# Performance work log

Hardware: AMD Instinct MI355X
Metric: run time of the kernel (lower is better)

## Reference

```python
import jax, jax.numpy as jnp
import numpy as np

# dims / config (from init_kwargs)
B, N, D, H = 8, 512, 256, 8
M, K, R = 8, 16, 8            # n_slots basis graphs, slot_dim, kernel_rank
DH = D // H
SCALE = 1.0 / float(np.sqrt(D))
TAU_AFF, TAU_SLOT = 1.0, 1.0
GW_EPS, GW_SIGMA = 0.05, 1.0
GW_OUTER, GW_SINK, TOL = 3, 10, 1e-6
G_DIV_LAMBDA, USAGE_LAMBDA, EPS = 0.1, 0.01, 1e-8


def setup_inputs() -> dict:
    key = jax.random.key(0)
    ks = jax.random.split(key, 9)
    xav = lambda k, shp: jax.random.normal(k, shp, jnp.float32) * float(np.sqrt(2.0 / (shp[-2] + shp[-1])))
    return {
        "x_desc": jax.random.normal(ks[0], (B, N, D), jnp.float32),
        "x_name": jax.random.normal(ks[1], (B, N, D), jnp.float32),
        "W1": xav(ks[2], (2 * D, D)), "b1": jnp.zeros((D,), jnp.float32),
        "W2": xav(ks[3], (D, D)),     "b2": jnp.zeros((D,), jnp.float32),
        "Wp": xav(ks[4], (D, M)),     "bp": jnp.zeros((M,), jnp.float32),
        "U_param": xav(ks[5], (M, K, R)),
    }


def _forward(x_desc, x_name, W1, b1, W2, b2, Wp, bp, U_param):
    # fusion MLP: Linear -> ReLU -> Linear
    z = jnp.concatenate([x_desc, x_name], axis=-1)          # [B,N,2D]
    z = jax.nn.relu(z @ W1 + b1) @ W2 + b2                  # [B,N,D]

    # per-head l2-normalized affinity, no self loop
    zh = z.reshape(B, N, H, DH).transpose(0, 2, 1, 3)       # [B,H,N,DH]
    zh = zh / jnp.clip(jnp.linalg.norm(zh, axis=-1, keepdims=True), 1e-8)
    logits = jnp.einsum('bhnd,bhsd->bhns', zh, zh) * (SCALE / TAU_AFF)
    logits = jnp.where(jnp.eye(N, dtype=bool), -1e9, logits)
    P = jax.nn.softmax(logits, axis=-1)                     # [B,H,N,N]

    # normalize_affinity (symmetrize + row-stochastic) -> distance
    Pn = 0.5 * (P + P.swapaxes(-1, -2))
    Pn = jnp.clip(Pn, EPS)
    Pn = Pn / jnp.clip(Pn.sum(-1, keepdims=True), EPS)
    DP = jnp.clip(1.0 - Pn, 0.0)                            # [B,H,N,N]

    # slot graphs G = softplus(U) softplus(U)^T, row-stochastic (kernel_row_stoch)
    U = jax.nn.softplus(U_param)                            # [M,K,R]
    G = jnp.einsum('mkr,mjr->mkj', U, U)                    # [M,K,K]
    G = G / jnp.clip(G.sum(-1, keepdims=True), EPS)

    # Frobenius diversity reg across the M graphs
    V = G.reshape(M, -1)
    V = V / jnp.clip(jnp.linalg.norm(V, axis=1, keepdims=True), 1e-8)
    Gram = V @ V.T
    g_reg = G_DIV_LAMBDA * (Gram.sum() - jnp.trace(Gram)) / (M * (M - 1))

    # cosine slot cost -> DG [M,K,K], zero diagonal
    diag = jnp.clip(jnp.diagonal(G, axis1=-2, axis2=-1), EPS)      # [M,K]
    denom = jnp.clip(jnp.sqrt(diag[:, :, None] * diag[:, None, :]), EPS)
    DG = jnp.clip(1.0 - jnp.clip(G / denom, -1.0, 1.0), 0.0)
    DG = DG * (1.0 - jnp.eye(K, dtype=DG.dtype))

    # entropic Gromov-Wasserstein between DP (nodes) and each DG_m (slots),
    # vectorized over the M graphs. a uniform over N, b uniform over K.
    Dx2, Dy2 = DP ** 2, DG ** 2
    a_w, b_w = 1.0 / N, 1.0 / K
    Pi = jnp.full((B, H, M, N, K), a_w * b_w, jnp.float32)

    def sinkhorn(C):
        Kmat = jnp.clip(jnp.exp(-C / GW_EPS), 1e-12)
        def body(i, uv):
            u, v = uv
            u = a_w / (jnp.einsum('bhmnk,bhmk->bhmn', Kmat, v) + TOL)
            v = b_w / (jnp.einsum('bhmnk,bhmn->bhmk', Kmat, u) + TOL)
            return (u, v)
        u0 = jnp.full((B, H, M, N), 1.0 / N, jnp.float32)
        v0 = jnp.full((B, H, M, K), 1.0 / K, jnp.float32)
        u, v = jax.lax.fori_loop(0, GW_SINK, body, (u0, v0))
        return u[..., :, None] * Kmat * v[..., None, :]

    C = None
    for _ in range(GW_OUTER):
        mass_j = Pi.sum(-1)                                  # [B,H,M,N]
        mass_l = Pi.sum(-2)                                  # [B,H,M,K]
        term1 = jnp.einsum('bhij,bhmj->bhmi', Dx2, mass_j)[..., :, None]
        term2 = jnp.einsum('mkl,bhml->bhmk', Dy2, mass_l)[..., None, :]
        cross = jnp.einsum('bhij,bhmjl,mkl->bhmik', DP, Pi, DG)
        C = jnp.clip(term1 + term2 - 2.0 * cross, 0.0)       # [B,H,M,N,K]
        Pi = sinkhorn(C)
    gw_val = (C * Pi).sum((-2, -1))                          # [B,H,M]

    # alpha weights over M graphs (alpha_from_gw)
    scores = jnp.exp(-(gw_val / GW_SIGMA) ** 2)
    alpha = scores / jnp.clip(scores.sum(-1, keepdims=True), 1e-8)

    # transport slot graphs back to node space, alpha-mix, row-normalize
    T = jnp.einsum('bhmnk,mkl->bhmnl', Pi, G)                # [B,H,M,N,K]
    Qmix = jnp.einsum('bhm,bhmnl,bhmsl->bhns', alpha, T, Pi)
    Qmix = jnp.clip(Qmix, EPS)
    Q = Qmix / Qmix.sum(-1, keepdims=True)                   # [B,H,N,N]
    bias_log = jnp.log(jax.lax.stop_gradient(Q))             # detached log-prior

    # slot usage regularizer (KL to uniform over M)
    A = jax.nn.softmax((z @ Wp + bp) / TAU_SLOT, axis=-1)     # [B,N,M]
    usage = A.mean((0, 1))
    usage_kl = jnp.sum(usage * jnp.log(jnp.clip(usage, EPS) * M))
    total_reg = g_reg + USAGE_LAMBDA * usage_kl
    return bias_log, Q, total_reg


def reference(x_desc, x_name, W1, b1, W2, b2, Wp, bp, U_param):
    return _forward(x_desc, x_name, W1, b1, W2, b2, Wp, bp, U_param)
```

## Files before the change

### kernel.cpp

```cpp
#include <hip/hip_runtime.h>
#include <cstdint>
#include <cstddef>

#define NB 8
#define NN 512
#define ND 256
#define NH 8
#define NM 8
#define NK 16
#define NR 8
#define NDH 32
#define BN (NB*NN)
#define BH (NB*NH)
#define BHN (BH*NN)
#define BHM (BH*NM)
#define QOFF 16777216

typedef __attribute__((ext_vector_type(8))) short bf16x8;
typedef __attribute__((ext_vector_type(8))) unsigned short u16x8;
typedef __attribute__((ext_vector_type(4))) float f32x4;

__device__ inline unsigned short f2bf(float x) {
  union { float f; unsigned u; } c; c.f = x;
  unsigned r = c.u + 0x7FFFu + ((c.u >> 16) & 1u);
  return (unsigned short)(r >> 16);
}
__device__ inline float bf2f(unsigned short x) {
  union { unsigned u; float f; } c; c.u = ((unsigned)x) << 16; return c.f;
}
__device__ inline float bflo(unsigned w2) {
  union { unsigned u; float f; } c; c.u = w2 << 16; return c.f;
}
__device__ inline float bfhi(unsigned w2) {
  union { unsigned u; float f; } c; c.u = w2 & 0xFFFF0000u; return c.f;
}

__global__ __launch_bounds__(256) void k_mlp1(const float* __restrict__ xd, const float* __restrict__ xn,
                       const float* __restrict__ W1, const float* __restrict__ b1,
                       float* __restrict__ hid) {
  __shared__ float As[16][68];
  __shared__ float Bs[16][68];
  int t = threadIdx.x;
  int col0 = blockIdx.x * 64;
  int row0 = blockIdx.y * 64;
  int ar = t >> 2, ak = (t & 3) * 4;
  int bk = t >> 4, bc = (t & 15) * 4;
  int ty = t >> 4, tx = t & 15;
  float acc[4][4] = {};
  for (int k0 = 0; k0 < 2*ND; k0 += 16) {
    int gk = k0 + ak;
    const float* src = (gk < ND) ? (xd + (size_t)(row0+ar)*ND + gk)
                                 : (xn + (size_t)(row0+ar)*ND + (gk-ND));
    float4 av = *(const float4*)src;
    As[ak+0][ar] = av.x; As[ak+1][ar] = av.y; As[ak+2][ar] = av.z; As[ak+3][ar] = av.w;
    float4 bv = *(const float4*)(W1 + (size_t)(k0+bk)*ND + col0 + bc);
    *(float4*)&Bs[bk][bc] = bv;
    __syncthreads();
    #pragma unroll
    for (int kk = 0; kk < 16; kk++) {
      float4 a = *(const float4*)&As[kk][ty*4];
      float4 b = *(const float4*)&Bs[kk][tx*4];
      acc[0][0] += a.x*b.x; acc[0][1] += a.x*b.y; acc[0][2] += a.x*b.z; acc[0][3] += a.x*b.w;
      acc[1][0] += a.y*b.x; acc[1][1] += a.y*b.y; acc[1][2] += a.y*b.z; acc[1][3] += a.y*b.w;
      acc[2][0] += a.z*b.x; acc[2][1] += a.z*b.y; acc[2][2] += a.z*b.z; acc[2][3] += a.z*b.w;
      acc[3][0] += a.w*b.x; acc[3][1] += a.w*b.y; acc[3][2] += a.w*b.z; acc[3][3] += a.w*b.w;
    }
    __syncthreads();
  }
  float4 bb = *(const float4*)(b1 + col0 + tx*4);
  #pragma unroll
  for (int a = 0; a < 4; a++) {
    float4 o;
    o.x = fmaxf(acc[a][0] + bb.x, 0.f);
    o.y = fmaxf(acc[a][1] + bb.y, 0.f);
    o.z = fmaxf(acc[a][2] + bb.z, 0.f);
    o.w = fmaxf(acc[a][3] + bb.w, 0.f);
    *(float4*)(hid + (size_t)(row0+ty*4+a)*ND + col0 + tx*4) = o;
  }
}

__global__ __launch_bounds__(256) void k_mlp2(const float* __restrict__ hidp,
                       const float* __restrict__ W2, const float* __restrict__ b2,
                       float* __restrict__ z) {
  __shared__ float As[16][68];
  __shared__ float Bs[16][68];
  int t = threadIdx.x;
  int col0 = blockIdx.x * 64;
  int row0 = blockIdx.y * 64;
  int ar = t >> 2, ak = (t & 3) * 4;
  int bk = t >> 4, bc = (t & 15) * 4;
  int ty = t >> 4, tx = t & 15;
  float acc[4][4] = {};
  for (int k0 = 0; k0 < ND; k0 += 16) {
    float4 av = *(const float4*)(hidp + (size_t)(row0+ar)*ND + k0 + ak);
    As[ak+0][ar] = av.x; As[ak+1][ar] = av.y; As[ak+2][ar] = av.z; As[ak+3][ar] = av.w;
    float4 bv = *(const float4*)(W2 + (size_t)(k0+bk)*ND + col0 + bc);
    *(float4*)&Bs[bk][bc] = bv;
    __syncthreads();
    #pragma unroll
    for (int kk = 0; kk < 16; kk++) {
      float4 a = *(const float4*)&As[kk][ty*4];
      float4 b = *(const float4*)&Bs[kk][tx*4];
      acc[0][0] += a.x*b.x; acc[0][1] += a.x*b.y; acc[0][2] += a.x*b.z; acc[0][3] += a.x*b.w;
      acc[1][0] += a.y*b.x; acc[1][1] += a.y*b.y; acc[1][2] += a.y*b.z; acc[1][3] += a.y*b.w;
      acc[2][0] += a.z*b.x; acc[2][1] += a.z*b.y; acc[2][2] += a.z*b.z; acc[2][3] += a.z*b.w;
      acc[3][0] += a.w*b.x; acc[3][1] += a.w*b.y; acc[3][2] += a.w*b.z; acc[3][3] += a.w*b.w;
    }
    __syncthreads();
  }
  float4 bb = *(const float4*)(b2 + col0 + tx*4);
  #pragma unroll
  for (int a = 0; a < 4; a++) {
    float4 o;
    o.x = acc[a][0] + bb.x; o.y = acc[a][1] + bb.y;
    o.z = acc[a][2] + bb.z; o.w = acc[a][3] + bb.w;
    *(float4*)(z + (size_t)(row0+ty*4+a)*ND + col0 + tx*4) = o;
  }
}

__global__ void k_zhnorm(const float* __restrict__ z, float* __restrict__ zh) {
  int idx = blockIdx.x*256 + threadIdx.x;
  int d = idx & 31;
  int n = (idx >> 5) & (NN-1);
  int h = (idx >> 14) & (NH-1);
  int b = idx >> 17;
  float v = z[(size_t)(b*NN + n)*ND + h*NDH + d];
  float ss = v*v;
  #pragma unroll
  for (int m = 1; m < 32; m <<= 1) ss += __shfl_xor(ss, m);
  zh[idx] = v / fmaxf(sqrtf(ss), 1e-8f);
}

__global__ __launch_bounds__(256) void k_affinity(const float* __restrict__ zh, unsigned short* __restrict__ P) {
  int blk = blockIdx.x;
  int rt = blk & 15, bh = blk >> 4;
  int r0 = rt*32;
  const float* base = zh + (size_t)bh*NN*NDH;
  __shared__ float qs[32][33];
  __shared__ float ks[32][36];
  int t = threadIdx.x;
  int sr = t >> 3, dq = (t & 7)*4;
  {
    float4 v = *(const float4*)(base + (size_t)(r0+sr)*NDH + dq);
    qs[sr][dq] = v.x; qs[sr][dq+1] = v.y; qs[sr][dq+2] = v.z; qs[sr][dq+3] = v.w;
  }
  int cr = t >> 3;
  int cq = t & 7;
  float acc[16][4];
  #pragma unroll
  for (int ti = 0; ti < 16; ti++) { acc[ti][0]=0; acc[ti][1]=0; acc[ti][2]=0; acc[ti][3]=0; }
  for (int ti = 0; ti < 16; ti++) {
    int s0 = ti*32;
    __syncthreads();
    {
      float4 v = *(const float4*)(base + (size_t)(s0+sr)*NDH + dq);
      ks[dq+0][sr] = v.x; ks[dq+1][sr] = v.y; ks[dq+2][sr] = v.z; ks[dq+3][sr] = v.w;
    }
    __syncthreads();
    #pragma unroll
    for (int d = 0; d < 32; d++) {
      float qv = qs[cr][d];
      float4 kv = *(const float4*)&ks[d][cq*4];
      acc[ti][0] += qv*kv.x; acc[ti][1] += qv*kv.y;
      acc[ti][2] += qv*kv.z; acc[ti][3] += qv*kv.w;
    }
  }
  int gr = r0 + cr;
  float mx = -1e30f;
  #pragma unroll
  for (int ti = 0; ti < 16; ti++) {
    #pragma unroll
    for (int j = 0; j < 4; j++) {
      int s = ti*32 + cq*4 + j;
      float v = (s == gr) ? -1e9f : acc[ti][j]*0.0625f;
      acc[ti][j] = v;
      mx = fmaxf(mx, v);
    }
  }
  mx = fmaxf(mx, __shfl_xor(mx, 1));
  mx = fmaxf(mx, __shfl_xor(mx, 2));
  mx = fmaxf(mx, __shfl_xor(mx, 4));
  float sum = 0.f;
  #pragma unroll
  for (int ti = 0; ti < 16; ti++) {
    #pragma unroll
    for (int j = 0; j < 4; j++) { float e = expf(acc[ti][j]-mx); acc[ti][j] = e; sum += e; }
  }
  sum += __shfl_xor(sum,1); sum += __shfl_xor(sum,2); sum += __shfl_xor(sum,4);
  float inv = 1.f/sum;
  unsigned short* prow = P + ((size_t)(bh*NN) + gr)*NN;
  #pragma unroll
  for (int ti = 0; ti < 16; ti++) {
    uint2 pk;
    pk.x = (unsigned)f2bf(acc[ti][0]*inv) | ((unsigned)f2bf(acc[ti][1]*inv) << 16);
    pk.y = (unsigned)f2bf(acc[ti][2]*inv) | ((unsigned)f2bf(acc[ti][3]*inv) << 16);
    *(uint2*)(prow + ti*32 + cq*4) = pk;
  }
}

__global__ __launch_bounds__(256) void k_dp(const unsigned short* __restrict__ P,
                       unsigned short* __restrict__ DPo, unsigned short* __restrict__ DPq,
                       float* __restrict__ rs, float* __restrict__ rq) {
  int blk = blockIdx.x;
  int rt = blk & 15, bh = blk >> 4;
  int r0 = rt*32;
  const unsigned short* Pb = P + (size_t)bh*NN*NN;
  __shared__ float Bs[32][33];
  int t = threadIdx.x;
  int r = t >> 3, q4 = (t & 7)*4;
  float pn[16][4];
  float rowacc = 0.f;
  for (int ti = 0; ti < 16; ti++) {
    int s0 = ti*32;
    __syncthreads();
    {
      uint2 v = *(const uint2*)(Pb + (size_t)(s0+r)*NN + r0 + q4);
      Bs[r][q4+0] = bf2f((unsigned short)(v.x & 0xFFFF));
      Bs[r][q4+1] = bf2f((unsigned short)(v.x >> 16));
      Bs[r][q4+2] = bf2f((unsigned short)(v.y & 0xFFFF));
      Bs[r][q4+3] = bf2f((unsigned short)(v.y >> 16));
    }
    uint2 av = *(const uint2*)(Pb + (size_t)(r0+r)*NN + s0 + q4);
    __syncthreads();
    float a0 = bf2f((unsigned short)(av.x & 0xFFFF));
    float a1 = bf2f((unsigned short)(av.x >> 16));
    float a2 = bf2f((unsigned short)(av.y & 0xFFFF));
    float a3 = bf2f((unsigned short)(av.y >> 16));
    float p0 = fmaxf(0.5f*(a0 + Bs[q4+0][r]), 1e-8f);
    float p1 = fmaxf(0.5f*(a1 + Bs[q4+1][r]), 1e-8f);
    float p2 = fmaxf(0.5f*(a2 + Bs[q4+2][r]), 1e-8f);
    float p3 = fmaxf(0.5f*(a3 + Bs[q4+3][r]), 1e-8f);
    pn[ti][0]=p0; pn[ti][1]=p1; pn[ti][2]=p2; pn[ti][3]=p3;
    rowacc += p0+p1+p2+p3;
  }
  rowacc += __shfl_xor(rowacc,1); rowacc += __shfl_xor(rowacc,2); rowacc += __shfl_xor(rowacc,4);
  float inv = 1.f / fmaxf(rowacc, 1e-8f);
  unsigned short* drow = DPo + ((size_t)(bh*NN) + r0 + r)*NN;
  unsigned short* qrow = DPq + ((size_t)(bh*NN) + r0 + r)*NN;
  float rsv = 0.f, rqv = 0.f;
  #pragma unroll
  for (int ti = 0; ti < 16; ti++) {
    float o0 = fmaxf(1.f - pn[ti][0]*inv, 0.f);
    float o1 = fmaxf(1.f - pn[ti][1]*inv, 0.f);
    float o2 = fmaxf(1.f - pn[ti][2]*inv, 0.f);
    float o3 = fmaxf(1.f - pn[ti][3]*inv, 0.f);
    rsv += o0+o1+o2+o3;
    rqv += o0*o0 + o1*o1 + o2*o2 + o3*o3;
    uint2 pk;
    pk.x = (unsigned)f2bf(o0) | ((unsigned)f2bf(o1) << 16);
    pk.y = (unsigned)f2bf(o2) | ((unsigned)f2bf(o3) << 16);
    *(uint2*)(drow + ti*32 + q4) = pk;
    uint2 qk;
    qk.x = (unsigned)f2bf(o0*o0) | ((unsigned)f2bf(o1*o1) << 16);
    qk.y = (unsigned)f2bf(o2*o2) | ((unsigned)f2bf(o3*o3) << 16);
    *(uint2*)(qrow + ti*32 + q4) = qk;
  }
  rsv += __shfl_xor(rsv,1); rsv += __shfl_xor(rsv,2); rsv += __shfl_xor(rsv,4);
  rqv += __shfl_xor(rqv,1); rqv += __shfl_xor(rqv,2); rqv += __shfl_xor(rqv,4);
  if ((t & 7) == 0) {
    rs[bh*NN + r0 + r] = rsv;
    rq[bh*NN + r0 + r] = rqv;
  }
}

__global__ void k_slots(const float* __restrict__ Up, float* __restrict__ G,
                        float* __restrict__ DG, float* __restrict__ greg) {
  __shared__ float U[NM*NK*NR];
  __shared__ float Gs[NM*NK*NK];
  __shared__ float rsx[NM*NK];
  __shared__ float vn[NM];
  __shared__ float gram[NM*NM];
  int t = threadIdx.x;
  for (int i = t; i < NM*NK*NR; i += 256) {
    float x = Up[i];
    U[i] = fmaxf(x, 0.f) + log1pf(expf(-fabsf(x)));
  }
  __syncthreads();
  for (int i = t; i < NM*NK*NK; i += 256) {
    int m = i >> 8, k = (i >> 4) & 15, j = i & 15;
    float acc = 0.f;
    #pragma unroll
    for (int r = 0; r < NR; r++) acc += U[(m*NK+k)*NR + r]*U[(m*NK+j)*NR + r];
    Gs[i] = acc;
  }
  __syncthreads();
  for (int i = t; i < NM*NK; i += 256) {
    float s = 0.f;
    #pragma unroll
    for (int j = 0; j < NK; j++) s += Gs[i*NK + j];
    rsx[i] = fmaxf(s, 1e-8f);
  }
  __syncthreads();
  for (int i = t; i < NM*NK*NK; i += 256) { Gs[i] /= rsx[i >> 4]; G[i] = Gs[i]; }
  __syncthreads();
  for (int i = t; i < NM; i += 256) {
    float s = 0.f;
    for (int j = 0; j < NK*NK; j++) { float g = Gs[i*NK*NK + j]; s += g*g; }
    vn[i] = fmaxf(sqrtf(s), 1e-8f);
  }
  __syncthreads();
  for (int i = t; i < NM*NM; i += 256) {
    int a = i >> 3, b = i & 7;
    float s = 0.f;
    for (int j = 0; j < NK*NK; j++) s += Gs[a*NK*NK + j]*Gs[b*NK*NK + j];
    gram[i] = s / (vn[a]*vn[b]);
  }
  __syncthreads();
  if (t == 0) {
    float s = 0.f;
    for (int i = 0; i < NM*NM; i++) if ((i >> 3) != (i & 7)) s += gram[i];
    greg[0] = 0.1f * s / (float)(NM*(NM-1));
  }
  for (int i = t; i < NM*NK*NK; i += 256) {
    int m = i >> 8, k = (i >> 4) & 15, j = i & 15;
    float dk = fmaxf(Gs[m*NK*NK + k*NK + k], 1e-8f);
    float dj = fmaxf(Gs[m*NK*NK + j*NK + j], 1e-8f);
    float den = fmaxf(sqrtf(dk*dj), 1e-8f);
    float c = fminf(fmaxf(Gs[i]/den, -1.f), 1.f);
    float d = fmaxf(1.f - c, 0.f);
    if (k == j) d = 0.f;
    DG[i] = d;
  }
}

#define DSTR 40
#define KST 522
#define PSTR 520
__global__ __launch_bounds__(512, 4) void k_gw(
    const unsigned short* __restrict__ DPb,
    const unsigned short* __restrict__ DPq,
    const float* __restrict__ rs, const float* __restrict__ rq,
    const float* __restrict__ Gm, const float* __restrict__ DGm,
    unsigned short* __restrict__ PiGs, unsigned short* __restrict__ Pis,
    float* __restrict__ gwv) {
  int blk = blockIdx.x;
  int xcd = blk & 7, seq = blk >> 3;
  int bh = xcd*8 + (seq >> 3);
  int m  = seq & 7;
  __shared__ __align__(16) unsigned short DPs[512*DSTR];
  __shared__ __align__(16) unsigned short KT[16*KST];
  __shared__ __align__(16) unsigned short PiT[16*PSTR];
  __shared__ __align__(16) float u[512];
  __shared__ __align__(16) float vv[16];
  __shared__ float ml[16], t2s[16], dgrow[16];
  __shared__ float Gsm[16][17], DGsm[16][17];
  __shared__ float sred[8][16];
  int t = threadIdx.x;
  int lane = t & 63, w = t >> 6;
  int il = lane & 15, q = lane >> 4;
  int g = t >> 4, kc = t & 15;
  if (t < 256) { Gsm[t>>4][t&15] = Gm[m*256 + t]; DGsm[t>>4][t&15] = DGm[m*256 + t]; }
  __syncthreads();
  if (t < 16) {
    float s = 0.f;
    #pragma unroll
    for (int l = 0; l < 16; l++) s += DGsm[t][l];
    dgrow[t] = s;
  }
  const unsigned short* DPbase = DPb + (size_t)bh*NN*NN;
  const unsigned short* DQbase = DPq + (size_t)bh*NN*NN;
  float rsv = rs[bh*NN + t]*(1.f/8192.f);
  float rqv = rq[bh*NN + t]*(1.f/512.f);
  float Kt[16];
  float creg[4][4];
  float ut = 0.f;
  int r0i = t >> 2, ci = (t & 3)*8;
  for (int itr = 0; itr < 3; ++itr) {
    if (t < 16) {
      float s = 0.f;
      #pragma unroll
      for (int l = 0; l < 16; l++) { float d = DGsm[t][l]; s += d*d*((itr == 0) ? (1.f/16.f) : ml[l]); }
      t2s[t] = s;
    }
    __syncthreads();
    if (itr == 0) {
      #pragma unroll
      for (int k = 0; k < 16; k++) {
        float c = fmaxf(rqv + t2s[k] - 2.f*rsv*dgrow[k], 0.f);
        float e = fmaxf(__expf(-20.f*c), 1e-12f);
        Kt[k] = e;
        KT[k*KST + t] = f2bf(e);
      }
    } else {
      f32x4 aW0={0,0,0,0}, aW1={0,0,0,0}, aW2={0,0,0,0}, aW3={0,0,0,0};
      f32x4 aV0={0,0,0,0}, aV1={0,0,0,0}, aV2={0,0,0,0}, aV3={0,0,0,0};
      float4 c0, c1, c2, c3;
      c0 = *(const float4*)(DPbase + (size_t)r0i*NN + ci);
      c1 = *(const float4*)(DPbase + (size_t)(r0i+128)*NN + ci);
      c2 = *(const float4*)(DPbase + (size_t)(r0i+256)*NN + ci);
      c3 = *(const float4*)(DPbase + (size_t)(r0i+384)*NN + ci);
      for (int p = 0; p < 16; p++) {
        *(float4*)&DPs[r0i*DSTR + ci] = c0;
        *(float4*)&DPs[(r0i+128)*DSTR + ci] = c1;
        *(float4*)&DPs[(r0i+256)*DSTR + ci] = c2;
        *(float4*)&DPs[(r0i+384)*DSTR + ci] = c3;
        __syncthreads();
        {
          const unsigned short* src = (p < 15) ? (DPbase + (p+1)*32) : DQbase;
          c0 = *(const float4*)(src + (size_t)r0i*NN + ci);
          c1 = *(const float4*)(src + (size_t)(r0i+128)*NN + ci);
          c2 = *(const float4*)(src + (size_t)(r0i+256)*NN + ci);
          c3 = *(const float4*)(src + (size_t)(r0i+384)*NN + ci);
        }
        bf16x8 af = *(const bf16x8*)&PiT[il*PSTR + p*32 + q*8];
        bf16x8 b0 = *(const bf16x8*)&DPs[(w*64 + il)*DSTR + q*8];
        bf16x8 b1 = *(const bf16x8*)&DPs[(w*64 + 16 + il)*DSTR + q*8];
        bf16x8 b2 = *(const bf16x8*)&DPs[(w*64 + 32 + il)*DSTR + q*8];
        bf16x8 b3 = *(const bf16x8*)&DPs[(w*64 + 48 + il)*DSTR + q*8];
        aW0 = __builtin_amdgcn_mfma_f32_16x16x32_bf16(af, b0, aW0, 0, 0, 0);
        aW1 = __builtin_amdgcn_mfma_f32_16x16x32_bf16(af, b1, aW1, 0, 0, 0);
        aW2 = __builtin_amdgcn_mfma_f32_16x16x32_bf16(af, b2, aW2, 0, 0, 0);
        aW3 = __builtin_amdgcn_mfma_f32_16x16x32_bf16(af, b3, aW3, 0, 0, 0);
        __syncthreads();
      }
      for (int p = 0; p < 16; p++) {
        *(float4*)&DPs[r0i*DSTR + ci] = c0;
        *(float4*)&DPs[(r0i+128)*DSTR + ci] = c1;
        *(float4*)&DPs[(r0i+256)*DSTR + ci] = c2;
        *(float4*)&DPs[(r0i+384)*DSTR + ci] = c3;
        __syncthreads();
        if (p < 15) {
          const unsigned short* src = DQbase + (p+1)*32;
          c0 = *(const float4*)(src + (size_t)r0i*NN + ci);
          c1 = *(const float4*)(src + (size_t)(r0i+128)*NN + ci);
          c2 = *(const float4*)(src + (size_t)(r0i+256)*NN + ci);
          c3 = *(const float4*)(src + (size_t)(r0i+384)*NN + ci);
        }
        bf16x8 af = *(const bf16x8*)&PiT[il*PSTR + p*32 + q*8];
        bf16x8 b0 = *(const bf16x8*)&DPs[(w*64 + il)*DSTR + q*8];
        bf16x8 b1 = *(const bf16x8*)&DPs[(w*64 + 16 + il)*DSTR + q*8];
        bf16x8 b2 = *(const bf16x8*)&DPs[(w*64 + 32 + il)*DSTR + q*8];
        bf16x8 b3 = *(const bf16x8*)&DPs[(w*64 + 48 + il)*DSTR + q*8];
        aV0 = __builtin_amdgcn_mfma_f32_16x16x32_bf16(af, b0, aV0, 0, 0, 0);
        aV1 = __builtin_amdgcn_mfma_f32_16x16x32_bf16(af, b1, aV1, 0, 0, 0);
        aV2 = __builtin_amdgcn_mfma_f32_16x16x32_bf16(af, b2, aV2, 0, 0, 0);
        aV3 = __builtin_amdgcn_mfma_f32_16x16x32_bf16(af, b3, aV3, 0, 0, 0);
        __syncthreads();
      }
      #pragma unroll
      for (int tt = 0; tt < 4; tt++) {
        f32x4 av = (tt==0)?aW0:((tt==1)?aW1:((tt==2)?aW2:aW3));
        f32x4 bv = (tt==0)?aV0:((tt==1)?aV1:((tt==2)?aV2:aV3));
        float tv = bv[0]+bv[1]+bv[2]+bv[3];
        tv += __shfl_xor(tv, 16); tv += __shfl_xor(tv, 32);
        float pc[16];
        #pragma unroll
        for (int k = 0; k < 16; k++) {
          pc[k] = av[0]*DGsm[k][q*4+0] + av[1]*DGsm[k][q*4+1]
                + av[2]*DGsm[k][q*4+2] + av[3]*DGsm[k][q*4+3];
        }
        #pragma unroll
        for (int k = 0; k < 16; k++) { pc[k] += __shfl_xor(pc[k], 16); pc[k] += __shfl_xor(pc[k], 32); }
        int i = w*64 + tt*16 + il;
        #pragma unroll
        for (int kk = 0; kk < 4; kk++) {
          int k = q*4 + kk;
          float c = fmaxf(tv + t2s[k] - 2.f*pc[k], 0.f);
          creg[tt][kk] = c;
          KT[k*KST + i] = f2bf(fmaxf(__expf(-20.f*c), 1e-12f));
        }
      }
      __syncthreads();
      #pragma unroll
      for (int k = 0; k < 16; k++) Kt[k] = bf2f(KT[k*KST + t]);
    }
    __syncthreads();
    if (t < 16) vv[t] = 1.f/16.f;
    __syncthreads();
    for (int si = 0; si < 10; si++) {
      float4 va = *(const float4*)&vv[0];
      float4 vb = *(const float4*)&vv[4];
      float4 vc = *(const float4*)&vv[8];
      float4 vd = *(const float4*)&vv[12];
      float s = Kt[0]*va.x + Kt[1]*va.y + Kt[2]*va.z + Kt[3]*va.w
              + Kt[4]*vb.x + Kt[5]*vb.y + Kt[6]*vb.z + Kt[7]*vb.w
              + Kt[8]*vc.x + Kt[9]*vc.y + Kt[10]*vc.z + Kt[11]*vc.w
              + Kt[12]*vd.x + Kt[13]*vd.y + Kt[14]*vd.z + Kt[15]*vd.w;
      ut = (1.f/512.f)/(s + 1e-6f);
      u[t] = ut;
      __syncthreads();
      const unsigned* kp = (const unsigned*)&KT[kc*KST + g*16];
      unsigned k0 = kp[0], k1 = kp[1], k2 = kp[2], k3 = kp[3];
      unsigned k4 = kp[4], k5 = kp[5], k6 = kp[6], k7 = kp[7];
      float4 ua = *(const float4*)&u[g*16];
      float4 ub = *(const float4*)&u[g*16+4];
      float4 uc = *(const float4*)&u[g*16+8];
      float4 ud = *(const float4*)&u[g*16+12];
      float p = bflo(k0)*ua.x + bfhi(k0)*ua.y + bflo(k1)*ua.z + bfhi(k1)*ua.w
              + bflo(k2)*ub.x + bfhi(k2)*ub.y + bflo(k3)*ub.z + bfhi(k3)*ub.w
              + bflo(k4)*uc.x + bfhi(k4)*uc.y + bflo(k5)*uc.z + bfhi(k5)*uc.w
              + bflo(k6)*ud.x + bfhi(k6)*ud.y + bflo(k7)*ud.z + bfhi(k7)*ud.w;
      p += __shfl_xor(p, 16); p += __shfl_xor(p, 32);
      if (lane < 16) sred[w][lane] = p;
      __syncthreads();
      if (t < 16) {
        float S = sred[0][t]+sred[1][t]+sred[2][t]+sred[3][t]
                + sred[4][t]+sred[5][t]+sred[6][t]+sred[7][t];
        float nv = (1.f/16.f)/(S + 1e-6f);
        vv[t] = nv;
        ml[t] = nv*S;
      }
      __syncthreads();
    }
    if (itr < 2) {
      const unsigned* kp = (const unsigned*)&KT[kc*KST + g*16];
      float4 ua = *(const float4*)&u[g*16];
      float4 ub = *(const float4*)&u[g*16+4];
      float4 uc = *(const float4*)&u[g*16+8];
      float4 ud = *(const float4*)&u[g*16+12];
      float vk = vv[kc];
      unsigned* pp = (unsigned*)&PiT[kc*PSTR + g*16];
      unsigned kx;
      kx = kp[0]; pp[0] = (unsigned)f2bf(ua.x*bflo(kx)*vk) | ((unsigned)f2bf(ua.y*bfhi(kx)*vk) << 16);
      kx = kp[1]; pp[1] = (unsigned)f2bf(ua.z*bflo(kx)*vk) | ((unsigned)f2bf(ua.w*bfhi(kx)*vk) << 16);
      kx = kp[2]; pp[2] = (unsigned)f2bf(ub.x*bflo(kx)*vk) | ((unsigned)f2bf(ub.y*bfhi(kx)*vk) << 16);
      kx = kp[3]; pp[3] = (unsigned)f2bf(ub.z*bflo(kx)*vk) | ((unsigned)f2bf(ub.w*bfhi(kx)*vk) << 16);
      kx = kp[4]; pp[4] = (unsigned)f2bf(uc.x*bflo(kx)*vk) | ((unsigned)f2bf(uc.y*bfhi(kx)*vk) << 16);
      kx = kp[5]; pp[5] = (unsigned)f2bf(uc.z*bflo(kx)*vk) | ((unsigned)f2bf(uc.w*bfhi(kx)*vk) << 16);
      kx = kp[6]; pp[6] = (unsigned)f2bf(ud.x*bflo(kx)*vk) | ((unsigned)f2bf(ud.y*bfhi(kx)*vk) << 16);
      kx = kp[7]; pp[7] = (unsigned)f2bf(ud.z*bflo(kx)*vk) | ((unsigned)f2bf(ud.w*bfhi(kx)*vk) << 16);
      __syncthreads();
    } else {
      float4 va = *(const float4*)&vv[0];
      float4 vb = *(const float4*)&vv[4];
      float4 vc = *(const float4*)&vv[8];
      float4 vd = *(const float4*)&vv[12];
      float vr[16] = {va.x,va.y,va.z,va.w, vb.x,vb.y,vb.z,vb.w,
                      vc.x,vc.y,vc.z,vc.w, vd.x,vd.y,vd.z,vd.w};
      float pi[16];
      #pragma unroll
      for (int k = 0; k < 16; k++) pi[k] = ut*Kt[k]*vr[k];
      size_t ob = ((size_t)bh*NN + t)*128 + m*16;
      {
        uint4 w0, w1;
        w0.x = (unsigned)f2bf(pi[0])  | ((unsigned)f2bf(pi[1])  << 16);
        w0.y = (unsigned)f2bf(pi[2])  | ((unsigned)f2bf(pi[3])  << 16);
        w0.z = (unsigned)f2bf(pi[4])  | ((unsigned)f2bf(pi[5])  << 16);
        w0.w = (unsigned)f2bf(pi[6])  | ((unsigned)f2bf(pi[7])  << 16);
        w1.x = (unsigned)f2bf(pi[8])  | ((unsigned)f2bf(pi[9])  << 16);
        w1.y = (unsigned)f2bf(pi[10]) | ((unsigned)f2bf(pi[11]) << 16);
        w1.z = (unsigned)f2bf(pi[12]) | ((unsigned)f2bf(pi[13]) << 16);
        w1.w = (unsigned)f2bf(pi[14]) | ((unsigned)f2bf(pi[15]) << 16);
        *(uint4*)(Pis + ob) = w0;
        *(uint4*)(Pis + ob + 8) = w1;
      }
      float pig[16];
      #pragma unroll
      for (int l = 0; l < 16; l++) {
        float s = 0.f;
        #pragma unroll
        for (int k = 0; k < 16; k++) s += pi[k]*Gsm[k][l];
        pig[l] = s;
      }
      {
        uint4 w0, w1;
        w0.x = (unsigned)f2bf(pig[0])  | ((unsigned)f2bf(pig[1])  << 16);
        w0.y = (unsigned)f2bf(pig[2])  | ((unsigned)f2bf(pig[3])  << 16);
        w0.z = (unsigned)f2bf(pig[4])  | ((unsigned)f2bf(pig[5])  << 16);
        w0.w = (unsigned)f2bf(pig[6])  | ((unsigned)f2bf(pig[7])  << 16);
        w1.x = (unsigned)f2bf(pig[8])  | ((unsigned)f2bf(pig[9])  << 16);
        w1.y = (unsigned)f2bf(pig[10]) | ((unsigned)f2bf(pig[11]) << 16);
        w1.z = (unsigned)f2bf(pig[12]) | ((unsigned)f2bf(pig[13]) << 16);
        w1.w = (unsigned)f2bf(pig[14]) | ((unsigned)f2bf(pig[15]) << 16);
        *(uint4*)(PiGs + ob) = w0;
        *(uint4*)(PiGs + ob + 8) = w1;
      }
      float gwp = 0.f;
      #pragma unroll
      for (int tt = 0; tt < 4; tt++) {
        int i = w*64 + tt*16 + il;
        float ui = u[i];
        #pragma unroll
        for (int kk = 0; kk < 4; kk++) {
          int k = q*4 + kk;
          gwp += creg[tt][kk]*(ui*bf2f(KT[k*KST + i])*vr[k]);
        }
      }
      #pragma unroll
      for (int off = 1; off < 64; off <<= 1) gwp += __shfl_xor(gwp, off);
      if (lane == 0) sred[w][0] = gwp;
      __syncthreads();
      if (t == 0) {
        float S = 0.f;
        #pragma unroll
        for (int w2 = 0; w2 < 8; w2++) S += sred[w2][0];
        gwv[bh*8 + m] = S;
      }
    }
  }
}

__global__ void k_alpha(const float* __restrict__ gw, float* __restrict__ alpha) {
  int t = threadIdx.x;
  float gg = gw[t];
  float sc = expf(-(gg*gg));
  float s = sc;
  s += __shfl_xor(s, 1); s += __shfl_xor(s, 2); s += __shfl_xor(s, 4);
  alpha[t] = sc / fmaxf(s, 1e-8f);
}

__global__ __launch_bounds__(256) void k_qgemm(const unsigned short* __restrict__ PiGs,
                       const unsigned short* __restrict__ Pis, const float* __restrict__ alpha,
                       float* __restrict__ out) {
  int bid = blockIdx.x;
  int blk = (bid & 7)*128 + (bid >> 3);
  int strip = blk & 15, bh = blk >> 4;
  int i0 = strip*32;
  __shared__ unsigned short As[32*128];
  __shared__ unsigned short Bs[128*128];
  __shared__ float rsum[4][32];
  __shared__ float als[8];
  int t = threadIdx.x;
  int w = t >> 6, lane = t & 63;
  if (t < 8) als[t] = alpha[bh*8 + t];
  __syncthreads();
  const unsigned short* Ab = PiGs + ((size_t)bh*NN + i0)*128;
  #pragma unroll
  for (int q = 0; q < 2; q++) {
    int idx = q*256 + t;
    int r = idx >> 4, sg = idx & 15;
    float4 v = *(const float4*)(Ab + r*128 + sg*8);
    u16x8 hv = *(u16x8*)&v;
    float a = als[sg >> 1];
    u16x8 o;
    #pragma unroll
    for (int e = 0; e < 8; e++) o[e] = f2bf(bf2f(hv[e])*a);
    *(u16x8*)&As[r*128 + (sg ^ (r & 7))*8] = o;
  }
  f32x4 acc[4][2][2] = {};
  const unsigned short* Bb = Pis + (size_t)bh*NN*128;
  for (int c = 0; c < 4; c++) {
    __syncthreads();
    #pragma unroll
    for (int q = 0; q < 8; q++) {
      int idx = q*256 + t;
      int r = idx >> 4, sg = idx & 15;
      float4 v = *(const float4*)(Bb + (size_t)(c*128 + r)*128 + sg*8);
      *(float4*)&Bs[r*128 + (sg ^ (r & 7))*8] = v;
    }
    __syncthreads();
    int col0 = w*32;
    #pragma unroll
    for (int ks = 0; ks < 4; ks++) {
      int slot = (ks*4 + (lane >> 4)) ^ (lane & 7);
      int la = lane & 15;
      bf16x8 a0 = *(bf16x8*)&As[la*128 + slot*8];
      bf16x8 a1 = *(bf16x8*)&As[(la+16)*128 + slot*8];
      bf16x8 b0 = *(bf16x8*)&Bs[(col0+la)*128 + slot*8];
      bf16x8 b1 = *(bf16x8*)&Bs[(col0+la+16)*128 + slot*8];
      acc[c][0][0] = __builtin_amdgcn_mfma_f32_16x16x32_bf16(a0, b0, acc[c][0][0], 0, 0, 0);
      acc[c][1][0] = __builtin_amdgcn_mfma_f32_16x16x32_bf16(a1, b0, acc[c][1][0], 0, 0, 0);
      acc[c][0][1] = __builtin_amdgcn_mfma_f32_16x16x32_bf16(a0, b1, acc[c][0][1], 0, 0, 0);
      acc[c][1][1] = __builtin_amdgcn_mfma_f32_16x16x32_bf16(a1, b1, acc[c][1][1], 0, 0, 0);
    }
  }
  float part[2][4];
  #pragma unroll
  for (int mt = 0; mt < 2; mt++) {
    #pragma unroll
    for (int rg = 0; rg < 4; rg++) {
      float s = 0.f;
      #pragma unroll
      for (int c = 0; c < 4; c++) {
        #pragma unroll
        for (int nt = 0; nt < 2; nt++) s += fmaxf(acc[c][mt][nt][rg], 1e-8f);
      }
      s += __shfl_xor(s, 1); s += __shfl_xor(s, 2);
      s += __shfl_xor(s, 4); s += __shfl_xor(s, 8);
      part[mt][rg] = s;
    }
  }
  if ((lane & 15) == 0) {
    int rgrp = lane >> 4;
    #pragma unroll
    for (int mt = 0; mt < 2; mt++)
      #pragma unroll
      for (int rg = 0; rg < 4; rg++)
        rsum[w][mt*16 + rgrp*4 + rg] = part[mt][rg];
  }
  __syncthreads();
  float invr[2][4];
  #pragma unroll
  for (int mt = 0; mt < 2; mt++) {
    #pragma unroll
    for (int rg = 0; rg < 4; rg++) {
      int row = mt*16 + (lane >> 4)*4 + rg;
      invr[mt][rg] = 1.f / (rsum[0][row] + rsum[1][row] + rsum[2][row] + rsum[3][row]);
    }
  }
  float* Qb = out + (size_t)QOFF + ((size_t)bh*NN + i0)*NN;
  float* Lb = out + ((size_t)bh*NN + i0)*NN;
  #pragma unroll
  for (int c = 0; c < 4; c++) {
    #pragma unroll
    for (int mt = 0; mt < 2; mt++) {
      #pragma unroll
      for (int nt = 0; nt < 2; nt++) {
        #pragma unroll
        for (int rg = 0; rg < 4; rg++) {
          int row = mt*16 + (lane >> 4)*4 + rg;
          int col = c*128 + w*32 + nt*16 + (lane & 15);
          float v = fmaxf(acc[c][mt][nt][rg], 1e-8f)*invr[mt][rg];
          Qb[(size_t)row*NN + col] = v;
          Lb[(size_t)row*NN + col] = __logf(v);
        }
      }
    }
  }
}

__global__ __launch_bounds__(256) void k_usage(const float* __restrict__ z, const float* __restrict__ Wp,
                        const float* __restrict__ bp, float* __restrict__ partial) {
  __shared__ float wps[256][9];
  __shared__ float red[256][8];
  int t = threadIdx.x;
  {
    float4 a = *(const float4*)(Wp + t*8);
    float4 b = *(const float4*)(Wp + t*8 + 4);
    wps[t][0]=a.x; wps[t][1]=a.y; wps[t][2]=a.z; wps[t][3]=a.w;
    wps[t][4]=b.x; wps[t][5]=b.y; wps[t][6]=b.z; wps[t][7]=b.w;
  }
  __syncthreads();
  int row = blockIdx.x*256 + t;
  const float* zr = z + (size_t)row*ND;
  float acc[8] = {};
  for (int d0 = 0; d0 < ND; d0 += 4) {
    float4 v = *(const float4*)(zr + d0);
    #pragma unroll
    for (int m = 0; m < 8; m++) {
      acc[m] += v.x*wps[d0][m] + v.y*wps[d0+1][m] + v.z*wps[d0+2][m] + v.w*wps[d0+3][m];
    }
  }
  float mx = -1e30f;
  #pragma unroll
  for (int m = 0; m < 8; m++) { acc[m] += bp[m]; mx = fmaxf(mx, acc[m]); }
  float s = 0.f;
  #pragma unroll
  for (int m = 0; m < 8; m++) { acc[m] = expf(acc[m]-mx); s += acc[m]; }
  float inv = 1.f/s;
  #pragma unroll
  for (int m = 0; m < 8; m++) red[t][m] = acc[m]*inv;
  __syncthreads();
  for (int q = 128; q > 0; q >>= 1) {
    if (t < q) { for (int m = 0; m < 8; m++) red[t][m] += red[t+q][m]; }
    __syncthreads();
  }
  if (t < 8) partial[blockIdx.x*8 + t] = red[0][t];
}

__global__ void k_final(const float* __restrict__ greg, const float* __restrict__ partial,
                        float* __restrict__ out) {
  if (threadIdx.x == 0) {
    float us[8] = {};
    for (int b = 0; b < 16; b++)
      for (int m = 0; m < 8; m++) us[m] += partial[b*8 + m];
    float kl = 0.f;
    for (int m = 0; m < 8; m++) {
      float u = us[m] / (float)BN;
      kl += u*logf(fmaxf(u, 1e-8f)*(float)NM);
    }
    out[33554432] = greg[0] + 0.01f*kl;
  }
}

extern "C" void kernel_launch(void* const* d_in, const int* in_sizes, int n_in,
                              void* d_out, int out_size, void* d_ws, size_t ws_size,
                              hipStream_t stream) {
  const float* xd = (const float*)d_in[0];
  const float* xn = (const float*)d_in[1];
  const float* W1 = (const float*)d_in[2];
  const float* b1 = (const float*)d_in[3];
  const float* W2 = (const float*)d_in[4];
  const float* b2 = (const float*)d_in[5];
  const float* Wp = (const float*)d_in[6];
  const float* bp = (const float*)d_in[7];
  const float* Up = (const float*)d_in[8];
  float* out = (float*)d_out;
  float* ws  = (float*)d_ws;

  float* z   = ws + 0;
  float* hid = ws + 1048576;
  float* zh  = ws + 2097152;
  unsigned short* PiGs = (unsigned short*)(ws + 3145728);
  unsigned short* Pis  = (unsigned short*)(ws + 5242880);
  float* gw    = ws + 7340032;
  float* alpha = ws + 7340544;
  float* G     = ws + 7341056;
  float* DG    = ws + 7343104;
  float* greg  = ws + 7345152;
  float* partial = ws + 7345153;
  float* rsb   = ws + 7345664;
  float* rqb   = ws + 7378432;

  unsigned short* P16 = (unsigned short*)out;
  unsigned short* DPb = (unsigned short*)(out + QOFF);
  unsigned short* DPq = DPb + (size_t)16777216;

  k_mlp1<<<dim3(4, 64), 256, 0, stream>>>(xd, xn, W1, b1, hid);
  k_mlp2<<<dim3(4, 64), 256, 0, stream>>>(hid, W2, b2, z);
  k_usage<<<16, 256, 0, stream>>>(z, Wp, bp, partial);
  k_zhnorm<<<4096, 256, 0, stream>>>(z, zh);
  k_affinity<<<1024, 256, 0, stream>>>(zh, P16);
  k_dp<<<1024, 256, 0, stream>>>(P16, DPb, DPq, rsb, rqb);
  k_slots<<<1, 256, 0, stream>>>(Up, G, DG, greg);
  k_gw<<<512, 512, 0, stream>>>(DPb, DPq, rsb, rqb, G, DG, PiGs, Pis, gw);
  k_alpha<<<1, 512, 0, stream>>>(gw, alpha);
  k_qgemm<<<1024, 256, 0, stream>>>(PiGs, Pis, alpha, out);
  k_final<<<1, 64, 0, stream>>>(greg, partial, out);
}
```

Measured before the change: 519.4 us.

## Store DP matrices in MFMA-fragment layout and load directly in GW kernel

Measured after the change: 508.5 us. 2.1% less time.

```diff
diff --git a/kernel.cpp b/kernel.cpp
--- a/kernel.cpp
+++ b/kernel.cpp
@@ -199,15 +199,19 @@
 }
 
 __global__ __launch_bounds__(256) void k_dp(const unsigned short* __restrict__ P,
-                       unsigned short* __restrict__ DPo, unsigned short* __restrict__ DPq,
+                       unsigned short* __restrict__ DPt, unsigned short* __restrict__ DQt,
                        float* __restrict__ rs, float* __restrict__ rq) {
   int blk = blockIdx.x;
   int rt = blk & 15, bh = blk >> 4;
   int r0 = rt*32;
   const unsigned short* Pb = P + (size_t)bh*NN*NN;
+  unsigned short* Dbase = DPt + (size_t)bh*NN*NN;
+  unsigned short* Qbase = DQt + (size_t)bh*NN*NN;
   __shared__ float Bs[32][33];
   int t = threadIdx.x;
   int r = t >> 3, q4 = (t & 7)*4;
+  int i = r0 + r;
+  int b = i >> 4, il = i & 15;
   float pn[16][4];
   float rowacc = 0.f;
   for (int ti = 0; ti < 16; ti++) {
@@ -220,7 +224,7 @@
       Bs[r][q4+2] = bf2f((unsigned short)(v.y & 0xFFFF));
       Bs[r][q4+3] = bf2f((unsigned short)(v.y >> 16));
     }
-    uint2 av = *(const uint2*)(Pb + (size_t)(r0+r)*NN + s0 + q4);
+    uint2 av = *(const uint2*)(Pb + (size_t)i*NN + s0 + q4);
     __syncthreads();
     float a0 = bf2f((unsigned short)(av.x & 0xFFFF));
     float a1 = bf2f((unsigned short)(av.x >> 16));
@@ -235,8 +239,6 @@
   }
   rowacc += __shfl_xor(rowacc,1); rowacc += __shfl_xor(rowacc,2); rowacc += __shfl_xor(rowacc,4);
   float inv = 1.f / fmaxf(rowacc, 1e-8f);
-  unsigned short* drow = DPo + ((size_t)(bh*NN) + r0 + r)*NN;
-  unsigned short* qrow = DPq + ((size_t)(bh*NN) + r0 + r)*NN;
   float rsv = 0.f, rqv = 0.f;
   #pragma unroll
   for (int ti = 0; ti < 16; ti++) {
@@ -246,20 +248,21 @@
     float o3 = fmaxf(1.f - pn[ti][3]*inv, 0.f);
     rsv += o0+o1+o2+o3;
     rqv += o0*o0 + o1*o1 + o2*o2 + o3*o3;
+    size_t fo = ((size_t)(ti*32 + b) << 9) + il*32 + q4;
     uint2 pk;
     pk.x = (unsigned)f2bf(o0) | ((unsigned)f2bf(o1) << 16);
     pk.y = (unsigned)f2bf(o2) | ((unsigned)f2bf(o3) << 16);
-    *(uint2*)(drow + ti*32 + q4) = pk;
+    *(uint2*)(Dbase + fo) = pk;
     uint2 qk;
     qk.x = (unsigned)f2bf(o0*o0) | ((unsigned)f2bf(o1*o1) << 16);
     qk.y = (unsigned)f2bf(o2*o2) | ((unsigned)f2bf(o3*o3) << 16);
-    *(uint2*)(qrow + ti*32 + q4) = qk;
+    *(uint2*)(Qbase + fo) = qk;
   }
   rsv += __shfl_xor(rsv,1); rsv += __shfl_xor(rsv,2); rsv += __shfl_xor(rsv,4);
   rqv += __shfl_xor(rqv,1); rqv += __shfl_xor(rqv,2); rqv += __shfl_xor(rqv,4);
   if ((t & 7) == 0) {
-    rs[bh*NN + r0 + r] = rsv;
-    rq[bh*NN + r0 + r] = rqv;
+    rs[bh*NN + i] = rsv;
+    rq[bh*NN + i] = rqv;
   }
 }
 
@@ -323,12 +326,11 @@
   }
 }
 
-#define DSTR 40
 #define KST 522
-#define PSTR 520
-__global__ __launch_bounds__(512, 4) void k_gw(
-    const unsigned short* __restrict__ DPb,
-    const unsigned short* __restrict__ DPq,
+#define PSTR 516
+__global__ __launch_bounds__(512, 2) void k_gw(
+    const unsigned short* __restrict__ DPt,
+    const unsigned short* __restrict__ DQt,
     const float* __restrict__ rs, const float* __restrict__ rq,
     const float* __restrict__ Gm, const float* __restrict__ DGm,
     unsigned short* __restrict__ PiGs, unsigned short* __restrict__ Pis,
@@ -337,7 +339,6 @@
   int xcd = blk & 7, seq = blk >> 3;
   int bh = xcd*8 + (seq >> 3);
   int m  = seq & 7;
-  __shared__ __align__(16) unsigned short DPs[512*DSTR];
   __shared__ __align__(16) unsigned short KT[16*KST];
   __shared__ __align__(16) unsigned short PiT[16*PSTR];
   __shared__ __align__(16) float u[512];
@@ -357,14 +358,13 @@
     for (int l = 0; l < 16; l++) s += DGsm[t][l];
     dgrow[t] = s;
   }
-  const unsigned short* DPbase = DPb + (size_t)bh*NN*NN;
-  const unsigned short* DQbase = DPq + (size_t)bh*NN*NN;
+  const unsigned short* Dbase = DPt + (size_t)bh*NN*NN;
+  const unsigned short* Qbase = DQt + (size_t)bh*NN*NN;
   float rsv = rs[bh*NN + t]*(1.f/8192.f);
   float rqv = rq[bh*NN + t]*(1.f/512.f);
   float Kt[16];
-  float creg[4][4];
   float ut = 0.f;
-  int r0i = t >> 2, ci = (t & 3)*8;
+  int lo = il*32 + q*8;
   for (int itr = 0; itr < 3; ++itr) {
     if (t < 16) {
       float s = 0.f;
@@ -384,58 +384,26 @@
     } else {
       f32x4 aW0={0,0,0,0}, aW1={0,0,0,0}, aW2={0,0,0,0}, aW3={0,0,0,0};
       f32x4 aV0={0,0,0,0}, aV1={0,0,0,0}, aV2={0,0,0,0}, aV3={0,0,0,0};
-      float4 c0, c1, c2, c3;
-      c0 = *(const float4*)(DPbase + (size_t)r0i*NN + ci);
-      c1 = *(const float4*)(DPbase + (size_t)(r0i+128)*NN + ci);
-      c2 = *(const float4*)(DPbase + (size_t)(r0i+256)*NN + ci);
-      c3 = *(const float4*)(DPbase + (size_t)(r0i+384)*NN + ci);
+      #pragma unroll 2
       for (int p = 0; p < 16; p++) {
-        *(float4*)&DPs[r0i*DSTR + ci] = c0;
-        *(float4*)&DPs[(r0i+128)*DSTR + ci] = c1;
-        *(float4*)&DPs[(r0i+256)*DSTR + ci] = c2;
-        *(float4*)&DPs[(r0i+384)*DSTR + ci] = c3;
-        __syncthreads();
-        {
-          const unsigned short* src = (p < 15) ? (DPbase + (p+1)*32) : DQbase;
-          c0 = *(const float4*)(src + (size_t)r0i*NN + ci);
-          c1 = *(const float4*)(src + (size_t)(r0i+128)*NN + ci);
-          c2 = *(const float4*)(src + (size_t)(r0i+256)*NN + ci);
-          c3 = *(const float4*)(src + (size_t)(r0i+384)*NN + ci);
-        }
         bf16x8 af = *(const bf16x8*)&PiT[il*PSTR + p*32 + q*8];
-        bf16x8 b0 = *(const bf16x8*)&DPs[(w*64 + il)*DSTR + q*8];
-        bf16x8 b1 = *(const bf16x8*)&DPs[(w*64 + 16 + il)*DSTR + q*8];
-        bf16x8 b2 = *(const bf16x8*)&DPs[(w*64 + 32 + il)*DSTR + q*8];
-        bf16x8 b3 = *(const bf16x8*)&DPs[(w*64 + 48 + il)*DSTR + q*8];
-        aW0 = __builtin_amdgcn_mfma_f32_16x16x32_bf16(af, b0, aW0, 0, 0, 0);
-        aW1 = __builtin_amdgcn_mfma_f32_16x16x32_bf16(af, b1, aW1, 0, 0, 0);
-        aW2 = __builtin_amdgcn_mfma_f32_16x16x32_bf16(af, b2, aW2, 0, 0, 0);
-        aW3 = __builtin_amdgcn_mfma_f32_16x16x32_bf16(af, b3, aW3, 0, 0, 0);
-        __syncthreads();
-      }
-      for (int p = 0; p < 16; p++) {
-        *(float4*)&DPs[r0i*DSTR + ci] = c0;
-        *(float4*)&DPs[(r0i+128)*DSTR + ci] = c1;
-        *(float4*)&DPs[(r0i+256)*DSTR + ci] = c2;
-        *(float4*)&DPs[(r0i+384)*DSTR + ci] = c3;
-        __syncthreads();
-        if (p < 15) {
-          const unsigned short* src = DQbase + (p+1)*32;
-          c0 = *(const float4*)(src + (size_t)r0i*NN + ci);
-          c1 = *(const float4*)(src + (size_t)(r0i+128)*NN + ci);
-          c2 = *(const float4*)(src + (size_t)(r0i+256)*NN + ci);
-          c3 = *(const float4*)(src + (size_t)(r0i+384)*NN + ci);
-        }
-        bf16x8 af = *(const bf16x8*)&PiT[il*PSTR + p*32 + q*8];
-        bf16x8 b0 = *(const bf16x8*)&DPs[(w*64 + il)*DSTR + q*8];
-        bf16x8 b1 = *(const bf16x8*)&DPs[(w*64 + 16 + il)*DSTR + q*8];
-        bf16x8 b2 = *(const bf16x8*)&DPs[(w*64 + 32 + il)*DSTR + q*8];
-        bf16x8 b3 = *(const bf16x8*)&DPs[(w*64 + 48 + il)*DSTR + q*8];
-        aV0 = __builtin_amdgcn_mfma_f32_16x16x32_bf16(af, b0, aV0, 0, 0, 0);
-        aV1 = __builtin_amdgcn_mfma_f32_16x16x32_bf16(af, b1, aV1, 0, 0, 0);
-        aV2 = __builtin_amdgcn_mfma_f32_16x16x32_bf16(af, b2, aV2, 0, 0, 0);
-        aV3 = __builtin_amdgcn_mfma_f32_16x16x32_bf16(af, b3, aV3, 0, 0, 0);
-        __syncthreads();
+        size_t fb = ((size_t)(p*32 + w*4) << 9) + lo;
+        bf16x8 w0 = *(const bf16x8*)(Dbase + fb);
+        bf16x8 w1 = *(const bf16x8*)(Dbase + fb + 512);
+        bf16x8 w2 = *(const bf16x8*)(Dbase + fb + 1024);
+        bf16x8 w3 = *(const bf16x8*)(Dbase + fb + 1536);
+        bf16x8 v0 = *(const bf16x8*)(Qbase + fb);
+        bf16x8 v1 = *(const bf16x8*)(Qbase + fb + 512);
+        bf16x8 v2 = *(const bf16x8*)(Qbase + fb + 1024);
+        bf16x8 v3 = *(const bf16x8*)(Qbase + fb + 1536);
+        aW0 = __builtin_amdgcn_mfma_f32_16x16x32_bf16(af, w0, aW0, 0, 0, 0);
+        aW1 = __builtin_amdgcn_mfma_f32_16x16x32_bf16(af, w1, aW1, 0, 0, 0);
+        aW2 = __builtin_amdgcn_mfma_f32_16x16x32_bf16(af, w2, aW2, 0, 0, 0);
+        aW3 = __builtin_amdgcn_mfma_f32_16x16x32_bf16(af, w3, aW3, 0, 0, 0);
+        aV0 = __builtin_amdgcn_mfma_f32_16x16x32_bf16(af, v0, aV0, 0, 0, 0);
+        aV1 = __builtin_amdgcn_mfma_f32_16x16x32_bf16(af, v1, aV1, 0, 0, 0);
+        aV2 = __builtin_amdgcn_mfma_f32_16x16x32_bf16(af, v2, aV2, 0, 0, 0);
+        aV3 = __builtin_amdgcn_mfma_f32_16x16x32_bf16(af, v3, aV3, 0, 0, 0);
       }
       #pragma unroll
       for (int tt = 0; tt < 4; tt++) {
@@ -456,7 +424,6 @@
         for (int kk = 0; kk < 4; kk++) {
           int k = q*4 + kk;
           float c = fmaxf(tv + t2s[k] - 2.f*pc[k], 0.f);
-          creg[tt][kk] = c;
           KT[k*KST + i] = f2bf(fmaxf(__expf(-20.f*c), 1e-12f));
         }
       }
@@ -528,8 +495,12 @@
       float vr[16] = {va.x,va.y,va.z,va.w, vb.x,vb.y,vb.z,vb.w,
                       vc.x,vc.y,vc.z,vc.w, vd.x,vd.y,vd.z,vd.w};
       float pi[16];
-      #pragma unroll
-      for (int k = 0; k < 16; k++) pi[k] = ut*Kt[k]*vr[k];
+      float gwp = 0.f;
+      #pragma unroll
+      for (int k = 0; k < 16; k++) {
+        pi[k] = ut*Kt[k]*vr[k];
+        gwp += (-0.05f*__logf(Kt[k]))*pi[k];
+      }
       size_t ob = ((size_t)bh*NN + t)*128 + m*16;
       {
         uint4 w0, w1;
@@ -564,17 +535,6 @@
         w1.w = (unsigned)f2bf(pig[14]) | ((unsigned)f2bf(pig[15]) << 16);
         *(uint4*)(PiGs + ob) = w0;
         *(uint4*)(PiGs + ob + 8) = w1;
-      }
-      float gwp = 0.f;
-      #pragma unroll
-      for (int tt = 0; tt < 4; tt++) {
-        int i = w*64 + tt*16 + il;
-        float ui = u[i];
-        #pragma unroll
-        for (int kk = 0; kk < 4; kk++) {
-          int k = q*4 + kk;
-          gwp += creg[tt][kk]*(ui*bf2f(KT[k*KST + i])*vr[k]);
-        }
       }
       #pragma unroll
       for (int off = 1; off < 64; off <<= 1) gwp += __shfl_xor(gwp, off);
@@ -793,17 +753,17 @@
   float* rqb   = ws + 7378432;
 
   unsigned short* P16 = (unsigned short*)out;
-  unsigned short* DPb = (unsigned short*)(out + QOFF);
-  unsigned short* DPq = DPb + (size_t)16777216;
+  unsigned short* DPt = (unsigned short*)(out + QOFF);
+  unsigned short* DQt = DPt + (size_t)16777216;
 
   k_mlp1<<<dim3(4, 64), 256, 0, stream>>>(xd, xn, W1, b1, hid);
   k_mlp2<<<dim3(4, 64), 256, 0, stream>>>(hid, W2, b2, z);
   k_usage<<<16, 256, 0, stream>>>(z, Wp, bp, partial);
   k_zhnorm<<<4096, 256, 0, stream>>>(z, zh);
   k_affinity<<<1024, 256, 0, stream>>>(zh, P16);
-  k_dp<<<1024, 256, 0, stream>>>(P16, DPb, DPq, rsb, rqb);
+  k_dp<<<1024, 256, 0, stream>>>(P16, DPt, DQt, rsb, rqb);
   k_slots<<<1, 256, 0, stream>>>(Up, G, DG, greg);
-  k_gw<<<512, 512, 0, stream>>>(DPb, DPq, rsb, rqb, G, DG, PiGs, Pis, gw);
+  k_gw<<<512, 512, 0, stream>>>(DPt, DQt, rsb, rqb, G, DG, PiGs, Pis, gw);
   k_alpha<<<1, 512, 0, stream>>>(gw, alpha);
   k_qgemm<<<1024, 256, 0, stream>>>(PiGs, Pis, alpha, out);
   k_final<<<1, 64, 0, stream>>>(greg, partial, out);
```
